# Kernel optimization log

Measured on AMD Instinct MI355X. Metric: run time of the kernel, lower is better.

Reference implementation:

```python
import jax, jax.numpy as jnp
import numpy as np

BATCH = 64
IN_VECN = 1024
IN_VECL = 64
OUT_VECN = 64
OUT_VECL = 32
ROUTINGS = 3
EPS = 1e-5


def squash(x, axis=-1, eps=EPS):
    # squash(x) = |x|^2/(1+|x|^2) * x/(|x|+eps), matching the torch source
    n = jnp.linalg.norm(x, axis=axis, keepdims=True)
    n2 = n * n
    return n2 / (1.0 + n2) * x / (n + eps)


def setup_inputs() -> dict:
    key = jax.random.key(0)
    k1, k2, k3 = jax.random.split(key, 3)
    stdv = 1.0 / np.sqrt(IN_VECN * IN_VECL)  # reset_parameters: uniform(-stdv, stdv)
    u = jax.random.normal(k1, (BATCH, IN_VECN, IN_VECL), dtype=jnp.float32)
    weight = jax.random.uniform(k2, (IN_VECN, OUT_VECN, OUT_VECL, IN_VECL),
                                dtype=jnp.float32, minval=-stdv, maxval=stdv)
    bias = jax.random.uniform(k3, (IN_VECN, OUT_VECN, OUT_VECL),
                              dtype=jnp.float32, minval=-stdv, maxval=stdv)
    return {"u": u, "weight": weight, "bias": bias}


def reference(u, weight, bias):
    # u: [B, N, I]; weight: [N, O, L, I]; bias: [N, O, L]
    # u_hat: [B, N, O, L] -- per-input-capsule prediction for each output capsule
    u_hat = jnp.einsum('bni,noli->bnol', u, weight) + bias[None]
    # retain_grad=False: routing uses detached u_hat
    ud = jax.lax.stop_gradient(u_hat)
    # initial c = softmax(zeros) over out_vecn -> uniform 1/O, shape [1,1,O,1]
    c = jnp.full((1, 1, OUT_VECN, 1), 1.0 / OUT_VECN, dtype=u.dtype)
    b = jnp.zeros((u.shape[0], IN_VECN, OUT_VECN, 1), dtype=u.dtype)
    for _ in range(ROUTINGS - 1):
        v = squash(jnp.sum(ud * c, axis=-3), axis=-1)        # [B, O, L]
        b = b + jnp.sum(ud * v[:, None], axis=-1, keepdims=True)  # [B, N, O, 1]
        c = jax.nn.softmax(b, axis=-2)                        # softmax over O
    return squash(jnp.sum(u_hat * c, axis=-3), axis=-1)      # [B, O, L]
```

## Files before the change

kernel.cpp:

```cpp
#include <hip/hip_runtime.h>

#define NIN 1024
#define IVL 64
#define ONUM 64
#define LVL 32
#define OLSZ 2048

typedef __attribute__((ext_vector_type(4))) float f32x4;
typedef __attribute__((ext_vector_type(4))) unsigned u32x4;
typedef __attribute__((ext_vector_type(8))) short short8;

static __device__ __forceinline__ unsigned short f2bf(float f) {
  unsigned u = __builtin_bit_cast(unsigned, f);
  u += 0x7fffu + ((u >> 16) & 1u);
  return (unsigned short)(u >> 16);
}
static __device__ __forceinline__ float bf2f_lo(unsigned x) {
  return __builtin_bit_cast(float, x << 16);
}
static __device__ __forceinline__ float bf2f_hi(unsigned x) {
  return __builtin_bit_cast(float, x & 0xffff0000u);
}

#define W_BURST16(W, q0, q1, q2, q3)                                     \
  asm volatile(                                                          \
      "global_load_dwordx4 %[w0], %[a0], off\n\t"                        \
      "global_load_dwordx4 %[w1], %[a0], off offset:16\n\t"              \
      "global_load_dwordx4 %[w2], %[a0], off offset:128\n\t"             \
      "global_load_dwordx4 %[w3], %[a0], off offset:144\n\t"             \
      "global_load_dwordx4 %[w4], %[a1], off\n\t"                        \
      "global_load_dwordx4 %[w5], %[a1], off offset:16\n\t"              \
      "global_load_dwordx4 %[w6], %[a1], off offset:128\n\t"             \
      "global_load_dwordx4 %[w7], %[a1], off offset:144\n\t"             \
      "global_load_dwordx4 %[w8], %[a2], off\n\t"                        \
      "global_load_dwordx4 %[w9], %[a2], off offset:16\n\t"              \
      "global_load_dwordx4 %[w10], %[a2], off offset:128\n\t"            \
      "global_load_dwordx4 %[w11], %[a2], off offset:144\n\t"            \
      "global_load_dwordx4 %[w12], %[a3], off\n\t"                       \
      "global_load_dwordx4 %[w13], %[a3], off offset:16\n\t"             \
      "global_load_dwordx4 %[w14], %[a3], off offset:128\n\t"            \
      "global_load_dwordx4 %[w15], %[a3], off offset:144\n\t"            \
      : [w0] "=&v"(W[0]), [w1] "=&v"(W[1]), [w2] "=&v"(W[2]),            \
        [w3] "=&v"(W[3]), [w4] "=&v"(W[4]), [w5] "=&v"(W[5]),            \
        [w6] "=&v"(W[6]), [w7] "=&v"(W[7]), [w8] "=&v"(W[8]),            \
        [w9] "=&v"(W[9]), [w10] "=&v"(W[10]), [w11] "=&v"(W[11]),        \
        [w12] "=&v"(W[12]), [w13] "=&v"(W[13]), [w14] "=&v"(W[14]),      \
        [w15] "=&v"(W[15])                                               \
      : [a0] "v"(q0), [a1] "v"(q1), [a2] "v"(q2), [a3] "v"(q3)           \
      : "memory")

#define VM_WAIT16                                       \
  do {                                                  \
    asm volatile("s_waitcnt vmcnt(16)" ::: "memory");   \
    __builtin_amdgcn_sched_barrier(0);                  \
  } while (0)
#define VM_WAIT8                                        \
  do {                                                  \
    asm volatile("s_waitcnt vmcnt(8)" ::: "memory");    \
    __builtin_amdgcn_sched_barrier(0);                  \
  } while (0)

#define TILE(W, TL, C, O0, O1, O2, O3, O4, O5, O6, O7)                        \
  do {                                                                        \
    const f32x4 A0 = (W)[(TL) * 4 + 0];                                       \
    const f32x4 A1 = (W)[(TL) * 4 + 1];                                       \
    const f32x4 A2 = (W)[(TL) * 4 + 2];                                       \
    const f32x4 A3 = (W)[(TL) * 4 + 3];                                       \
    short8 wf0, wf1;                                                          \
    wf0[0] = (short)f2bf(A0[0]); wf0[1] = (short)f2bf(A0[1]);                 \
    wf0[2] = (short)f2bf(A0[2]); wf0[3] = (short)f2bf(A0[3]);                 \
    wf0[4] = (short)f2bf(A1[0]); wf0[5] = (short)f2bf(A1[1]);                 \
    wf0[6] = (short)f2bf(A1[2]); wf0[7] = (short)f2bf(A1[3]);                 \
    wf1[0] = (short)f2bf(A2[0]); wf1[1] = (short)f2bf(A2[1]);                 \
    wf1[2] = (short)f2bf(A2[2]); wf1[3] = (short)f2bf(A2[3]);                 \
    wf1[4] = (short)f2bf(A3[0]); wf1[5] = (short)f2bf(A3[1]);                 \
    wf1[6] = (short)f2bf(A3[2]); wf1[7] = (short)f2bf(A3[3]);                 \
    float4 bf = *(const float4*)&bias_lds[wave * 256 + (C) * 64 + (TL) * 16 + \
                                          quad * 4];                          \
    f32x4 a0 = (f32x4){0.f, 0.f, 0.f, 0.f};                                   \
    f32x4 a1 = a0, a2 = a0, a3 = a0;                                          \
    a0 = __builtin_amdgcn_mfma_f32_16x16x32_bf16(wf0, uf[0][0], a0, 0, 0, 0); \
    a0 = __builtin_amdgcn_mfma_f32_16x16x32_bf16(wf1, uf[0][1], a0, 0, 0, 0); \
    a1 = __builtin_amdgcn_mfma_f32_16x16x32_bf16(wf0, uf[1][0], a1, 0, 0, 0); \
    a1 = __builtin_amdgcn_mfma_f32_16x16x32_bf16(wf1, uf[1][1], a1, 0, 0, 0); \
    a2 = __builtin_amdgcn_mfma_f32_16x16x32_bf16(wf0, uf[2][0], a2, 0, 0, 0); \
    a2 = __builtin_amdgcn_mfma_f32_16x16x32_bf16(wf1, uf[2][1], a2, 0, 0, 0); \
    a3 = __builtin_amdgcn_mfma_f32_16x16x32_bf16(wf0, uf[3][0], a3, 0, 0, 0); \
    a3 = __builtin_amdgcn_mfma_f32_16x16x32_bf16(wf1, uf[3][1], a3, 0, 0, 0); \
    O0 = f2bf(a0[0] + bf.x) | ((unsigned)f2bf(a0[1] + bf.y) << 16);           \
    O1 = f2bf(a0[2] + bf.z) | ((unsigned)f2bf(a0[3] + bf.w) << 16);           \
    O2 = f2bf(a1[0] + bf.x) | ((unsigned)f2bf(a1[1] + bf.y) << 16);           \
    O3 = f2bf(a1[2] + bf.z) | ((unsigned)f2bf(a1[3] + bf.w) << 16);           \
    O4 = f2bf(a2[0] + bf.x) | ((unsigned)f2bf(a2[1] + bf.y) << 16);           \
    O5 = f2bf(a2[2] + bf.z) | ((unsigned)f2bf(a2[3] + bf.w) << 16);           \
    O6 = f2bf(a3[0] + bf.x) | ((unsigned)f2bf(a3[1] + bf.y) << 16);           \
    O7 = f2bf(a3[2] + bf.z) | ((unsigned)f2bf(a3[3] + bf.w) << 16);           \
  } while (0)

#define STEP(W, C)                                                            \
  do {                                                                        \
    u32x4 kA0, kA1, kA2, kA3, kB0, kB1, kB2, kB3;                             \
    TILE(W, 0, C, kA0.x, kA0.y, kA1.x, kA1.y, kA2.x, kA2.y, kA3.x, kA3.y);    \
    TILE(W, 1, C, kA0.z, kA0.w, kA1.z, kA1.w, kA2.z, kA2.w, kA3.z, kA3.w);    \
    TILE(W, 2, C, kB0.x, kB0.y, kB1.x, kB1.y, kB2.x, kB2.y, kB3.x, kB3.y);    \
    TILE(W, 3, C, kB0.z, kB0.w, kB1.z, kB1.w, kB2.z, kB2.w, kB3.z, kB3.w);    \
    const unsigned short* c0 = sb0 + (C) * 64;                                \
    const unsigned short* c1 = sb1 + (C) * 64;                                \
    const unsigned short* c2 = sb2 + (C) * 64;                                \
    const unsigned short* c3 = sb3 + (C) * 64;                                \
    asm volatile(                                                             \
        "global_store_dwordx4 %[a0], %[d0], off\n\t"                          \
        "global_store_dwordx4 %[a0], %[d1], off offset:16\n\t"                \
        "global_store_dwordx4 %[a1], %[d2], off\n\t"                          \
        "global_store_dwordx4 %[a1], %[d3], off offset:16\n\t"                \
        "global_store_dwordx4 %[a2], %[d4], off\n\t"                          \
        "global_store_dwordx4 %[a2], %[d5], off offset:16\n\t"                \
        "global_store_dwordx4 %[a3], %[d6], off\n\t"                          \
        "global_store_dwordx4 %[a3], %[d7], off offset:16\n\t"                \
        :: [a0] "v"(c0), [a1] "v"(c1), [a2] "v"(c2), [a3] "v"(c3),            \
           [d0] "v"(kA0), [d1] "v"(kB0), [d2] "v"(kA1), [d3] "v"(kB1),        \
           [d4] "v"(kA2), [d5] "v"(kB2), [d6] "v"(kA3), [d7] "v"(kB3)         \
        : "memory");                                                          \
  } while (0)

__global__ __launch_bounds__(256, 2) void k_gemm(
    const float* __restrict__ u, const float* __restrict__ w,
    const float* __restrict__ bias, unsigned short* __restrict__ uhat,
    float* __restrict__ szero) {
  const int n = blockIdx.x;
  const int half = blockIdx.y;
  __shared__ __align__(16) unsigned short a_lds[64 * 72];
  __shared__ __align__(16) float bias_lds[1024];
  const int t = threadIdx.x;
  const int lane = t & 63;
  const int wave = t >> 6;
  const int row16 = lane & 15;
  const int quad = lane >> 4;

  {
    const int bid = half * 1024 + n;
    if (t < 192) szero[bid * 192 + t] = 0.f;
  }

  {
    const int b = t >> 2;
    const int i0 = (t & 3) * 16;
    const float* src = u + (size_t)b * (NIN * IVL) + (size_t)n * IVL + i0;
    unsigned short* dst = a_lds + b * 72 + i0;
#pragma unroll
    for (int q = 0; q < 4; ++q) {
      float4 v = *(const float4*)(src + q * 4);
      dst[q * 4 + 0] = f2bf(v.x);
      dst[q * 4 + 1] = f2bf(v.y);
      dst[q * 4 + 2] = f2bf(v.z);
      dst[q * 4 + 3] = f2bf(v.w);
    }
    *(float4*)&bias_lds[t * 4] =
        *(const float4*)(bias + (size_t)n * OLSZ + half * 1024 + t * 4);
  }

  const float* wp = w + (size_t)n * (OLSZ * IVL) +
                    (size_t)(half * 1024 + wave * 256 + row16) * IVL + quad * 8;
  f32x4 bufA[16], bufB[16];
  W_BURST16(bufA, wp, wp + 1024, wp + 2048, wp + 3072);
  W_BURST16(bufB, wp + 4096, wp + 5120, wp + 6144, wp + 7168);

  asm volatile("s_waitcnt lgkmcnt(0)" ::: "memory");
  __builtin_amdgcn_s_barrier();

  short8 uf[4][2];
#pragma unroll
  for (int bt = 0; bt < 4; ++bt) {
#pragma unroll
    for (int ks = 0; ks < 2; ++ks) {
      uf[bt][ks] =
          *(const short8*)(a_lds + (bt * 16 + row16) * 72 + ks * 32 + quad * 8);
    }
  }

  const unsigned short* sb0 = uhat + ((size_t)row16 * NIN + n) * OLSZ +
                              half * 1024 + wave * 256 + quad * 16;
  const unsigned short* sb1 = sb0 + (size_t)16 * NIN * OLSZ;
  const unsigned short* sb2 = sb0 + (size_t)32 * NIN * OLSZ;
  const unsigned short* sb3 = sb0 + (size_t)48 * NIN * OLSZ;

  VM_WAIT16; STEP(bufA, 0); W_BURST16(bufA, wp + 8192, wp + 9216, wp + 10240, wp + 11264);
  VM_WAIT16; STEP(bufB, 1); W_BURST16(bufB, wp + 12288, wp + 13312, wp + 14336, wp + 15360);
  VM_WAIT16; STEP(bufA, 2);
  VM_WAIT8;  STEP(bufB, 3);
}

__global__ __launch_bounds__(256) void k_sum_n(
    const unsigned short* __restrict__ uhat, float* __restrict__ s1) {
  const int b = blockIdx.x >> 5;
  const int chunk = blockIdx.x & 31;
  const int t = threadIdx.x;
  const unsigned short* base =
      uhat + ((size_t)b * NIN + (size_t)chunk * 32) * OLSZ + t * 8;
  float acc[8];
#pragma unroll
  for (int j = 0; j < 8; ++j) acc[j] = 0.f;
#pragma unroll 4
  for (int k = 0; k < 32; ++k) {
    uint4 p = *(const uint4*)(base + (size_t)k * OLSZ);
    unsigned xs[4] = {p.x, p.y, p.z, p.w};
#pragma unroll
    for (int h = 0; h < 4; ++h) {
      acc[2 * h] += bf2f_lo(xs[h]);
      acc[2 * h + 1] += bf2f_hi(xs[h]);
    }
  }
  float* s = s1 + (size_t)b * OLSZ + t * 8;
#pragma unroll
  for (int j = 0; j < 8; ++j) atomicAdd(s + j, acc[j]);
}

__global__ __launch_bounds__(256) void k_route(
    const unsigned short* __restrict__ uhat, const float* __restrict__ sv,
    float scale, float* __restrict__ b1, int add_b1,
    float* __restrict__ sout) {
  const int b = blockIdx.x >> 5;
  const int chunk = blockIdx.x & 31;
  const int t = threadIdx.x;
  const int lane = t & 63;
  const int wave = t >> 6;
  const int g2 = ((lane >> 3) << 1) | (lane & 1);
  __shared__ float red[4][OLSZ];

  float v[4][8];
#pragma unroll
  for (int q = 0; q < 4; ++q) {
    const float* svp = sv + (size_t)b * OLSZ + q * 512 + lane * 8;
    float4 a0 = *(const float4*)svp;
    float4 a1 = *(const float4*)(svp + 4);
    v[q][0] = a0.x * scale; v[q][1] = a0.y * scale;
    v[q][2] = a0.z * scale; v[q][3] = a0.w * scale;
    v[q][4] = a1.x * scale; v[q][5] = a1.y * scale;
    v[q][6] = a1.z * scale; v[q][7] = a1.w * scale;
    float p = 0.f;
#pragma unroll
    for (int j = 0; j < 8; ++j) p = fmaf(v[q][j], v[q][j], p);
    p += __shfl_xor(p, 2);
    p += __shfl_xor(p, 4);
    float f = p / ((1.f + p) * (sqrtf(p) + 1e-5f));
#pragma unroll
    for (int j = 0; j < 8; ++j) v[q][j] *= f;
  }

  float racc[4][8];
#pragma unroll
  for (int q = 0; q < 4; ++q)
#pragma unroll
    for (int j = 0; j < 8; ++j) racc[q][j] = 0.f;

  const int n0 = chunk * 32 + wave * 8;
  const unsigned short* ub = uhat + ((size_t)b * NIN + n0) * OLSZ + lane * 8;

  uint4 pA[4], pB[4];
#pragma unroll
  for (int q = 0; q < 4; ++q) pA[q] = *(const uint4*)(ub + q * 512);

  auto process = [&](const uint4(&pk)[4], int k) {
    const int n = n0 + k;
    const size_t bbase = ((size_t)b * NIN + n) * ONUM + g2;
    float b1v[4];
    if (add_b1) {
#pragma unroll
      for (int q = 0; q < 4; ++q) b1v[q] = b1[bbase + 16 * q];
    }
    float ud[4][8];
    float d[4];
#pragma unroll
    for (int q = 0; q < 4; ++q) {
      unsigned xs[4] = {pk[q].x, pk[q].y, pk[q].z, pk[q].w};
#pragma unroll
      for (int h = 0; h < 4; ++h) {
        ud[q][2 * h] = bf2f_lo(xs[h]);
        ud[q][2 * h + 1] = bf2f_hi(xs[h]);
      }
      float p = 0.f;
#pragma unroll
      for (int j = 0; j < 8; ++j) p = fmaf(ud[q][j], v[q][j], p);
      p += __shfl_xor(p, 2);
      p += __shfl_xor(p, 4);
      d[q] = p;
    }
    float bno[4];
    if (add_b1) {
#pragma unroll
      for (int q = 0; q < 4; ++q) bno[q] = d[q] + b1v[q];
    } else {
#pragma unroll
      for (int q = 0; q < 4; ++q) bno[q] = d[q];
      if ((lane & 6) == 0) {
#pragma unroll
        for (int q = 0; q < 4; ++q) b1[bbase + 16 * q] = d[q];
      }
    }
    float m = fmaxf(fmaxf(bno[0], bno[1]), fmaxf(bno[2], bno[3]));
    m = fmaxf(m, __shfl_xor(m, 1));
    m = fmaxf(m, __shfl_xor(m, 8));
    m = fmaxf(m, __shfl_xor(m, 16));
    m = fmaxf(m, __shfl_xor(m, 32));
    float e0 = __expf(bno[0] - m);
    float e1 = __expf(bno[1] - m);
    float e2 = __expf(bno[2] - m);
    float e3 = __expf(bno[3] - m);
    float ls = (e0 + e1) + (e2 + e3);
    ls += __shfl_xor(ls, 1);
    ls += __shfl_xor(ls, 8);
    ls += __shfl_xor(ls, 16);
    ls += __shfl_xor(ls, 32);
    float inv = 1.0f / ls;
    float c[4] = {e0 * inv, e1 * inv, e2 * inv, e3 * inv};
#pragma unroll
    for (int q = 0; q < 4; ++q) {
#pragma unroll
      for (int j = 0; j < 8; ++j)
        racc[q][j] = fmaf(c[q], ud[q][j], racc[q][j]);
    }
  };

#pragma unroll
  for (int kk = 0; kk < 4; ++kk) {
    {
#pragma unroll
      for (int q = 0; q < 4; ++q)
        pB[q] = *(const uint4*)(ub + (size_t)(2 * kk + 1) * OLSZ + q * 512);
    }
    process(pA, 2 * kk);
    if (2 * kk + 2 < 8) {
#pragma unroll
      for (int q = 0; q < 4; ++q)
        pA[q] = *(const uint4*)(ub + (size_t)(2 * kk + 2) * OLSZ + q * 512);
    }
    process(pB, 2 * kk + 1);
  }

#pragma unroll
  for (int q = 0; q < 4; ++q) {
    float* dst = &red[wave][q * 512 + lane * 8];
    *(float4*)(dst) =
        make_float4(racc[q][0], racc[q][1], racc[q][2], racc[q][3]);
    *(float4*)(dst + 4) =
        make_float4(racc[q][4], racc[q][5], racc[q][6], racc[q][7]);
  }
  __syncthreads();
  float* so = sout + (size_t)b * OLSZ;
#pragma unroll
  for (int j = 0; j < 8; ++j) {
    const int idx = t + 256 * j;
    float s = (red[0][idx] + red[1][idx]) + (red[2][idx] + red[3][idx]);
    atomicAdd(so + idx, s);
  }
}

__global__ __launch_bounds__(256) void k_final(const float* __restrict__ s3,
                                               float* __restrict__ out) {
  const int b = blockIdx.x;
  const int t = threadIdx.x;
  __shared__ float norm2[64];
  if (t < 64) norm2[t] = 0.f;
  __syncthreads();
  float scv[8];
#pragma unroll
  for (int k = 0; k < 8; ++k) {
    int idx = t + k * 256;
    float sc = s3[b * OLSZ + idx];
    scv[k] = sc;
    int o = ((idx >> 9) << 4) + (((idx >> 6) & 7) << 1) + ((idx >> 3) & 1);
    atomicAdd(&norm2[o], sc * sc);
  }
  __syncthreads();
#pragma unroll
  for (int k = 0; k < 8; ++k) {
    int idx = t + k * 256;
    int o = ((idx >> 9) << 4) + (((idx >> 6) & 7) << 1) + ((idx >> 3) & 1);
    float n2 = norm2[o];
    float f = n2 / ((1.f + n2) * (sqrtf(n2) + 1e-5f));
    int q2 = (idx >> 4) & 3;
    int t2 = (idx >> 2) & 3;
    int j = idx & 3;
    int fr = (idx & ~63) | (t2 << 4) | (q2 << 2) | j;
    out[b * OLSZ + fr] = scv[k] * f;
  }
}

extern "C" void kernel_launch(void* const* d_in, const int* in_sizes, int n_in,
                              void* d_out, int out_size, void* d_ws,
                              size_t ws_size, hipStream_t stream) {
  const float* u = (const float*)d_in[0];
  const float* w = (const float*)d_in[1];
  const float* bias = (const float*)d_in[2];
  float* out = (float*)d_out;

  char* ws = (char*)d_ws;
  unsigned short* uhat = (unsigned short*)ws;
  float* b1 = (float*)(ws + (size_t)268435456);
  float* s1 = (float*)(ws + (size_t)268435456 + 16777216);
  float* s2 = s1 + 131072;
  float* s3 = s2 + 131072;

  k_gemm<<<dim3(1024, 2), dim3(256), 0, stream>>>(u, w, bias, uhat, s1);
  k_sum_n<<<dim3(2048), dim3(256), 0, stream>>>(uhat, s1);
  k_route<<<dim3(2048), dim3(256), 0, stream>>>(uhat, s1, 1.0f / 64.0f, b1, 0, s2);
  k_route<<<dim3(2048), dim3(256), 0, stream>>>(uhat, s2, 1.0f, b1, 1, s3);
  k_final<<<dim3(64), dim3(256), 0, stream>>>(s3, out);
}
```

Measured before the change: 479.6 us.

## Recompute routing logits from summed squashed vectors and use nontemporal memory ops

The second routing pass no longer reads a stored b1 logit buffer. It computes the logits as u_hat·(v1+v2), using linearity of the dot product, so both squashed vectors are folded into a single v per block. This removes the b1 writes in the first pass and the b1 reads in the second pass, at the cost of loading and squashing a second s vector per block. Separately, the weight loads, the u_hat stores and the u_hat streaming loads now carry nontemporal hints to limit cache pollution.

After: 566.2 us. +18.0%, slower.

```diff
diff --git a/kernel.cpp b/kernel.cpp
--- a/kernel.cpp
+++ b/kernel.cpp
@@ -21,25 +21,28 @@
 static __device__ __forceinline__ float bf2f_hi(unsigned x) {
   return __builtin_bit_cast(float, x & 0xffff0000u);
 }
+static __device__ __forceinline__ u32x4 ntload4(const unsigned short* p) {
+  return __builtin_nontemporal_load((const u32x4*)p);
+}
 
 #define W_BURST16(W, q0, q1, q2, q3)                                     \
   asm volatile(                                                          \
-      "global_load_dwordx4 %[w0], %[a0], off\n\t"                        \
-      "global_load_dwordx4 %[w1], %[a0], off offset:16\n\t"              \
-      "global_load_dwordx4 %[w2], %[a0], off offset:128\n\t"             \
-      "global_load_dwordx4 %[w3], %[a0], off offset:144\n\t"             \
-      "global_load_dwordx4 %[w4], %[a1], off\n\t"                        \
-      "global_load_dwordx4 %[w5], %[a1], off offset:16\n\t"              \
-      "global_load_dwordx4 %[w6], %[a1], off offset:128\n\t"             \
-      "global_load_dwordx4 %[w7], %[a1], off offset:144\n\t"             \
-      "global_load_dwordx4 %[w8], %[a2], off\n\t"                        \
-      "global_load_dwordx4 %[w9], %[a2], off offset:16\n\t"              \
-      "global_load_dwordx4 %[w10], %[a2], off offset:128\n\t"            \
-      "global_load_dwordx4 %[w11], %[a2], off offset:144\n\t"            \
-      "global_load_dwordx4 %[w12], %[a3], off\n\t"                       \
-      "global_load_dwordx4 %[w13], %[a3], off offset:16\n\t"             \
-      "global_load_dwordx4 %[w14], %[a3], off offset:128\n\t"            \
-      "global_load_dwordx4 %[w15], %[a3], off offset:144\n\t"            \
+      "global_load_dwordx4 %[w0], %[a0], off nt\n\t"                     \
+      "global_load_dwordx4 %[w1], %[a0], off offset:16 nt\n\t"           \
+      "global_load_dwordx4 %[w2], %[a0], off offset:128 nt\n\t"          \
+      "global_load_dwordx4 %[w3], %[a0], off offset:144 nt\n\t"          \
+      "global_load_dwordx4 %[w4], %[a1], off nt\n\t"                     \
+      "global_load_dwordx4 %[w5], %[a1], off offset:16 nt\n\t"           \
+      "global_load_dwordx4 %[w6], %[a1], off offset:128 nt\n\t"          \
+      "global_load_dwordx4 %[w7], %[a1], off offset:144 nt\n\t"          \
+      "global_load_dwordx4 %[w8], %[a2], off nt\n\t"                     \
+      "global_load_dwordx4 %[w9], %[a2], off offset:16 nt\n\t"           \
+      "global_load_dwordx4 %[w10], %[a2], off offset:128 nt\n\t"         \
+      "global_load_dwordx4 %[w11], %[a2], off offset:144 nt\n\t"         \
+      "global_load_dwordx4 %[w12], %[a3], off nt\n\t"                    \
+      "global_load_dwordx4 %[w13], %[a3], off offset:16 nt\n\t"          \
+      "global_load_dwordx4 %[w14], %[a3], off offset:128 nt\n\t"         \
+      "global_load_dwordx4 %[w15], %[a3], off offset:144 nt\n\t"         \
       : [w0] "=&v"(W[0]), [w1] "=&v"(W[1]), [w2] "=&v"(W[2]),            \
         [w3] "=&v"(W[3]), [w4] "=&v"(W[4]), [w5] "=&v"(W[5]),            \
         [w6] "=&v"(W[6]), [w7] "=&v"(W[7]), [w8] "=&v"(W[8]),            \
@@ -109,14 +112,14 @@
     const unsigned short* c2 = sb2 + (C) * 64;                                \
     const unsigned short* c3 = sb3 + (C) * 64;                                \
     asm volatile(                                                             \
-        "global_store_dwordx4 %[a0], %[d0], off\n\t"                          \
-        "global_store_dwordx4 %[a0], %[d1], off offset:16\n\t"                \
-        "global_store_dwordx4 %[a1], %[d2], off\n\t"                          \
-        "global_store_dwordx4 %[a1], %[d3], off offset:16\n\t"                \
-        "global_store_dwordx4 %[a2], %[d4], off\n\t"                          \
-        "global_store_dwordx4 %[a2], %[d5], off offset:16\n\t"                \
-        "global_store_dwordx4 %[a3], %[d6], off\n\t"                          \
-        "global_store_dwordx4 %[a3], %[d7], off offset:16\n\t"                \
+        "global_store_dwordx4 %[a0], %[d0], off nt\n\t"                       \
+        "global_store_dwordx4 %[a0], %[d1], off offset:16 nt\n\t"             \
+        "global_store_dwordx4 %[a1], %[d2], off nt\n\t"                       \
+        "global_store_dwordx4 %[a1], %[d3], off offset:16 nt\n\t"             \
+        "global_store_dwordx4 %[a2], %[d4], off nt\n\t"                       \
+        "global_store_dwordx4 %[a2], %[d5], off offset:16 nt\n\t"             \
+        "global_store_dwordx4 %[a3], %[d6], off nt\n\t"                       \
+        "global_store_dwordx4 %[a3], %[d7], off offset:16 nt\n\t"             \
         :: [a0] "v"(c0), [a1] "v"(c1), [a2] "v"(c2), [a3] "v"(c3),            \
            [d0] "v"(kA0), [d1] "v"(kB0), [d2] "v"(kA1), [d3] "v"(kB1),        \
            [d4] "v"(kA2), [d5] "v"(kB2), [d6] "v"(kA3), [d7] "v"(kB3)         \
@@ -202,12 +205,11 @@
   for (int j = 0; j < 8; ++j) acc[j] = 0.f;
 #pragma unroll 4
   for (int k = 0; k < 32; ++k) {
-    uint4 p = *(const uint4*)(base + (size_t)k * OLSZ);
-    unsigned xs[4] = {p.x, p.y, p.z, p.w};
+    u32x4 p = ntload4(base + (size_t)k * OLSZ);
 #pragma unroll
     for (int h = 0; h < 4; ++h) {
-      acc[2 * h] += bf2f_lo(xs[h]);
-      acc[2 * h + 1] += bf2f_hi(xs[h]);
+      acc[2 * h] += bf2f_lo(p[h]);
+      acc[2 * h + 1] += bf2f_hi(p[h]);
     }
   }
   float* s = s1 + (size_t)b * OLSZ + t * 8;
@@ -216,27 +218,26 @@
 }
 
 __global__ __launch_bounds__(256) void k_route(
-    const unsigned short* __restrict__ uhat, const float* __restrict__ sv,
-    float scale, float* __restrict__ b1, int add_b1,
+    const unsigned short* __restrict__ uhat, const float* __restrict__ svA,
+    float scaleA, const float* __restrict__ svB, float scaleB, int useB,
     float* __restrict__ sout) {
   const int b = blockIdx.x >> 5;
   const int chunk = blockIdx.x & 31;
   const int t = threadIdx.x;
   const int lane = t & 63;
   const int wave = t >> 6;
-  const int g2 = ((lane >> 3) << 1) | (lane & 1);
   __shared__ float red[4][OLSZ];
 
   float v[4][8];
 #pragma unroll
   for (int q = 0; q < 4; ++q) {
-    const float* svp = sv + (size_t)b * OLSZ + q * 512 + lane * 8;
+    const float* svp = svA + (size_t)b * OLSZ + q * 512 + lane * 8;
     float4 a0 = *(const float4*)svp;
     float4 a1 = *(const float4*)(svp + 4);
-    v[q][0] = a0.x * scale; v[q][1] = a0.y * scale;
-    v[q][2] = a0.z * scale; v[q][3] = a0.w * scale;
-    v[q][4] = a1.x * scale; v[q][5] = a1.y * scale;
-    v[q][6] = a1.z * scale; v[q][7] = a1.w * scale;
+    v[q][0] = a0.x * scaleA; v[q][1] = a0.y * scaleA;
+    v[q][2] = a0.z * scaleA; v[q][3] = a0.w * scaleA;
+    v[q][4] = a1.x * scaleA; v[q][5] = a1.y * scaleA;
+    v[q][6] = a1.z * scaleA; v[q][7] = a1.w * scaleA;
     float p = 0.f;
 #pragma unroll
     for (int j = 0; j < 8; ++j) p = fmaf(v[q][j], v[q][j], p);
@@ -246,6 +247,27 @@
 #pragma unroll
     for (int j = 0; j < 8; ++j) v[q][j] *= f;
   }
+  if (useB) {
+#pragma unroll
+    for (int q = 0; q < 4; ++q) {
+      const float* svp = svB + (size_t)b * OLSZ + q * 512 + lane * 8;
+      float4 a0 = *(const float4*)svp;
+      float4 a1 = *(const float4*)(svp + 4);
+      float w2[8];
+      w2[0] = a0.x * scaleB; w2[1] = a0.y * scaleB;
+      w2[2] = a0.z * scaleB; w2[3] = a0.w * scaleB;
+      w2[4] = a1.x * scaleB; w2[5] = a1.y * scaleB;
+      w2[6] = a1.z * scaleB; w2[7] = a1.w * scaleB;
+      float p = 0.f;
+#pragma unroll
+      for (int j = 0; j < 8; ++j) p = fmaf(w2[j], w2[j], p);
+      p += __shfl_xor(p, 2);
+      p += __shfl_xor(p, 4);
+      float f = p / ((1.f + p) * (sqrtf(p) + 1e-5f));
+#pragma unroll
+      for (int j = 0; j < 8; ++j) v[q][j] = fmaf(w2[j], f, v[q][j]);
+    }
+  }
 
   float racc[4][8];
 #pragma unroll
@@ -256,27 +278,19 @@
   const int n0 = chunk * 32 + wave * 8;
   const unsigned short* ub = uhat + ((size_t)b * NIN + n0) * OLSZ + lane * 8;
 
-  uint4 pA[4], pB[4];
-#pragma unroll
-  for (int q = 0; q < 4; ++q) pA[q] = *(const uint4*)(ub + q * 512);
-
-  auto process = [&](const uint4(&pk)[4], int k) {
-    const int n = n0 + k;
-    const size_t bbase = ((size_t)b * NIN + n) * ONUM + g2;
-    float b1v[4];
-    if (add_b1) {
-#pragma unroll
-      for (int q = 0; q < 4; ++q) b1v[q] = b1[bbase + 16 * q];
-    }
+  u32x4 pA[4], pB[4];
+#pragma unroll
+  for (int q = 0; q < 4; ++q) pA[q] = ntload4(ub + q * 512);
+
+  auto process = [&](const u32x4(&pk)[4]) {
     float ud[4][8];
     float d[4];
 #pragma unroll
     for (int q = 0; q < 4; ++q) {
-      unsigned xs[4] = {pk[q].x, pk[q].y, pk[q].z, pk[q].w};
 #pragma unroll
       for (int h = 0; h < 4; ++h) {
-        ud[q][2 * h] = bf2f_lo(xs[h]);
-        ud[q][2 * h + 1] = bf2f_hi(xs[h]);
+        ud[q][2 * h] = bf2f_lo(pk[q][h]);
+        ud[q][2 * h + 1] = bf2f_hi(pk[q][h]);
       }
       float p = 0.f;
 #pragma unroll
@@ -285,27 +299,15 @@
       p += __shfl_xor(p, 4);
       d[q] = p;
     }
-    float bno[4];
-    if (add_b1) {
-#pragma unroll
-      for (int q = 0; q < 4; ++q) bno[q] = d[q] + b1v[q];
-    } else {
-#pragma unroll
-      for (int q = 0; q < 4; ++q) bno[q] = d[q];
-      if ((lane & 6) == 0) {
-#pragma unroll
-        for (int q = 0; q < 4; ++q) b1[bbase + 16 * q] = d[q];
-      }
-    }
-    float m = fmaxf(fmaxf(bno[0], bno[1]), fmaxf(bno[2], bno[3]));
+    float m = fmaxf(fmaxf(d[0], d[1]), fmaxf(d[2], d[3]));
     m = fmaxf(m, __shfl_xor(m, 1));
     m = fmaxf(m, __shfl_xor(m, 8));
     m = fmaxf(m, __shfl_xor(m, 16));
     m = fmaxf(m, __shfl_xor(m, 32));
-    float e0 = __expf(bno[0] - m);
-    float e1 = __expf(bno[1] - m);
-    float e2 = __expf(bno[2] - m);
-    float e3 = __expf(bno[3] - m);
+    float e0 = __expf(d[0] - m);
+    float e1 = __expf(d[1] - m);
+    float e2 = __expf(d[2] - m);
+    float e3 = __expf(d[3] - m);
     float ls = (e0 + e1) + (e2 + e3);
     ls += __shfl_xor(ls, 1);
     ls += __shfl_xor(ls, 8);
@@ -326,15 +328,15 @@
     {
 #pragma unroll
       for (int q = 0; q < 4; ++q)
-        pB[q] = *(const uint4*)(ub + (size_t)(2 * kk + 1) * OLSZ + q * 512);
-    }
-    process(pA, 2 * kk);
+        pB[q] = ntload4(ub + (size_t)(2 * kk + 1) * OLSZ + q * 512);
+    }
+    process(pA);
     if (2 * kk + 2 < 8) {
 #pragma unroll
       for (int q = 0; q < 4; ++q)
-        pA[q] = *(const uint4*)(ub + (size_t)(2 * kk + 2) * OLSZ + q * 512);
-    }
-    process(pB, 2 * kk + 1);
+        pA[q] = ntload4(ub + (size_t)(2 * kk + 2) * OLSZ + q * 512);
+    }
+    process(pB);
   }
 
 #pragma unroll
@@ -396,14 +398,15 @@
 
   char* ws = (char*)d_ws;
   unsigned short* uhat = (unsigned short*)ws;
-  float* b1 = (float*)(ws + (size_t)268435456);
-  float* s1 = (float*)(ws + (size_t)268435456 + 16777216);
+  float* s1 = (float*)(ws + (size_t)268435456);
   float* s2 = s1 + 131072;
   float* s3 = s2 + 131072;
 
   k_gemm<<<dim3(1024, 2), dim3(256), 0, stream>>>(u, w, bias, uhat, s1);
   k_sum_n<<<dim3(2048), dim3(256), 0, stream>>>(uhat, s1);
-  k_route<<<dim3(2048), dim3(256), 0, stream>>>(uhat, s1, 1.0f / 64.0f, b1, 0, s2);
-  k_route<<<dim3(2048), dim3(256), 0, stream>>>(uhat, s2, 1.0f, b1, 1, s3);
+  k_route<<<dim3(2048), dim3(256), 0, stream>>>(uhat, s1, 1.0f / 64.0f,
+                                                (const float*)nullptr, 0.f, 0, s2);
+  k_route<<<dim3(2048), dim3(256), 0, stream>>>(uhat, s1, 1.0f / 64.0f,
+                                                s2, 1.0f, 1, s3);
   k_final<<<dim3(64), dim3(256), 0, stream>>>(s3, out);
 }
```
